# Performance work log

Measured on AMD Instinct MI355X. Metric: run time of the kernel, lower is better.

## Reference

```python
import jax, jax.numpy as jnp
import numpy as np
from jax import lax

# fixed differential-operator kernel bank K() from SPDE_pac (8 channels of 3x3 stencils)
_K = np.zeros((8, 3, 3), np.float32)
_K[0, 1, 1] = 1.0
_K[1, 1, 1] = 2.0
_K[2, 1, 0] = -1.0; _K[2, 1, 2] = -1.0
_K[3, 1, 1] = 2.0
_K[4, 0, 1] = -1.0; _K[4, 2, 1] = -1.0
_K[5, 0, 0] = -0.5; _K[5, 2, 2] = -0.5; _K[5, 0, 2] = 0.5; _K[5, 2, 0] = 0.5
_K[6, 1, 0] = -1.0; _K[6, 1, 2] = 1.0
_K[7, 0, 1] = 1.0; _K[7, 2, 1] = -1.0
_KMAT = jnp.asarray(_K)


def _conv(x, w):
    # 3x3 same-padded conv, no bias (torch Conv2d padding=1, bias=False)
    return lax.conv_general_dilated(x, w, (1, 1), 'SAME',
                                    dimension_numbers=('NCHW', 'OIHW', 'NCHW'))


def _softplus10(x):
    return jax.nn.softplus(10.0 * x) / 10.0


def _forward(x, conv1_w, conv2_w, conv3_w, pac_w, pac_b):
    b, t, h, w = x.shape
    # ---- encode_param_CNN ----
    p = _conv(jax.nn.relu(x), conv1_w)
    p = _conv(jax.nn.relu(p), conv2_w)
    params = _conv(p, conv3_w)                       # [b, 6t, h, w]
    # ---- decode_param_CNN (kept in [b,t,h,w] layout; H = gamma*I + v v^T per pixel) ----
    kappa = _softplus10(params[:, :t])
    m1d = params[:, t:2 * t]                         # decoder m1 -> m[:,0]
    m2d = params[:, 2 * t:3 * t]                     # decoder m2 -> m[:,1]
    gamma = _softplus10(params[:, 3 * t:4 * t])
    vx = params[:, 4 * t:5 * t]
    vy = params[:, 5 * t:6 * t]
    H11 = gamma + vx * vx
    H22 = gamma + vy * vy
    H12 = vx * vy
    # ---- SPDE_pac kernel construction ----
    # guide channels as in source: (kappa, H11, 1/H11, H22, 1/H22, H12, m[:,1], m[:,0])
    guide = jnp.stack([kappa, H11, 1.0 / H11, H22, 1.0 / H22, H12, m2d, m1d], axis=2)  # [b,t,8,h,w]
    w_ker = jnp.einsum('ide,btihw->btdehw', _KMAT, guide)   # [b,t,3,3,h,w]
    w_ker = w_ker.at[:, :, 1, 1].add(1.0)                   # w_I identity-center kernel
    # ---- pixel-adaptive conv; loop over k is independent (reads x[:,k+1]) -> vectorize over time ----
    xin = x[:, 1:]                                          # [b,t-1,h,w]
    xp = jnp.pad(xin, ((0, 0), (0, 0), (1, 1), (1, 1)))
    patches = jnp.stack([xp[:, :, d:d + h, e:e + w]
                         for d in range(3) for e in range(3)], axis=2)  # [b,t-1,9,h,w]
    wflat = w_ker[:, 1:].reshape(b, t - 1, 9, h, w)
    out = jnp.einsum('k,btkhw,btkhw->bthw', pac_w.reshape(9), wflat, patches) + pac_b[0]
    # last time slice of x_spde is never written -> zeros
    return jnp.concatenate([out, jnp.zeros((b, 1, h, w), x.dtype)], axis=1)


def setup_inputs() -> dict:
    key = jax.random.key(0)
    ks = jax.random.split(key, 6)
    b, t, h, w = 4, 10, 256, 256
    dim_ae = 32
    x = jax.random.normal(ks[0], (b, t, h, w), jnp.float32)
    conv1_w = jax.random.normal(ks[1], (dim_ae, t, 3, 3), jnp.float32) * 0.05
    conv2_w = jax.random.normal(ks[2], (2 * dim_ae, dim_ae, 3, 3), jnp.float32) * 0.05
    conv3_w = jax.random.normal(ks[3], (6 * t, 2 * dim_ae, 3, 3), jnp.float32) * 0.05
    pac_w = jax.random.normal(ks[4], (1, 1, 3, 3), jnp.float32) * 0.2
    pac_b = jax.random.normal(ks[5], (1,), jnp.float32) * 0.1
    return {"x": x, "conv1_w": conv1_w, "conv2_w": conv2_w,
            "conv3_w": conv3_w, "pac_w": pac_w, "pac_b": pac_b}


def reference(x, conv1_w, conv2_w, conv3_w, pac_w, pac_b):
    return _forward(x, conv1_w, conv2_w, conv3_w, pac_w, pac_b)
```

## Files before the change

kernel.cpp:

```cpp
#include <hip/hip_runtime.h>
#include <math.h>

#define HH 256
#define WW 256
#define HW (HH * WW)
#define TB 10

typedef __attribute__((ext_vector_type(4))) float f32x4;
typedef __attribute__((ext_vector_type(8))) short s16x8;

__device__ __forceinline__ float sp10(float x) {
    float z = 10.0f * x;
    return (fmaxf(z, 0.0f) + log1pf(expf(-fabsf(z)))) * 0.1f;
}

__device__ __forceinline__ unsigned short f2bf(float f) {
    unsigned u = __float_as_uint(f);
    u = u + 0x7FFFu + ((u >> 16) & 1u);
    return (unsigned short)(u >> 16);
}
__device__ __forceinline__ void bsplit(float v, unsigned short& h, unsigned short& l) {
    h = f2bf(v);
    float hf = __uint_as_float(((unsigned)h) << 16);
    l = f2bf(v - hf);
}
__device__ __forceinline__ unsigned pk(unsigned short a, unsigned short b) {
    return (unsigned)a | ((unsigned)b << 16);
}
__device__ __forceinline__ void sp2(float a, float b, unsigned& uh, unsigned& ul) {
    unsigned short h1, l1, h2, l2;
    bsplit(a, h1, l1); bsplit(b, h2, l2);
    uh = pk(h1, h2); ul = pk(l1, l2);
}

__global__ __launch_bounds__(256) void prep_weights(
    const float* __restrict__ w1, const float* __restrict__ w2,
    const float* __restrict__ w3,
    float* __restrict__ wt1,
    unsigned short* __restrict__ wA2h, unsigned short* __restrict__ wA2l,
    unsigned short* __restrict__ wA3h, unsigned short* __restrict__ wA3l)
{
    int idx = blockIdx.x * 256 + threadIdx.x;
    if (idx < 2880) {
        int ci = idx / 288; int rem = idx - ci * 288;
        int tap = rem / 32; int co = rem - tap * 32;
        wt1[idx] = w1[co * 90 + ci * 9 + tap];
    }
    if (idx < 18432) {
        int t = idx / 2048; int rem = idx - t * 2048;
        int co = rem >> 5; int ci = rem & 31;
        unsigned short h, l;
        bsplit(w2[(co * 32 + ci) * 9 + t], h, l);
        wA2h[idx] = h; wA2l[idx] = l;
    }
    if (idx < 36864) {
        int t = idx / 4096; int rem = idx - t * 4096;
        int co = rem >> 6; int ci = rem & 63;
        float v = 0.0f;
        if (co < 54) {
            int tt = co / 6 + 1;
            int g  = co - (tt - 1) * 6;
            v = w3[((g * 10 + tt) * 64 + ci) * 9 + t];
        }
        unsigned short h, l;
        bsplit(v, h, l);
        wA3h[idx] = h; wA3l[idx] = l;
    }
}

__global__ __launch_bounds__(256, 4) void conv1_k(
    const float* __restrict__ x, const float* __restrict__ wt1,
    unsigned short* __restrict__ q1h, unsigned short* __restrict__ q1l)
{
    __shared__ float tile[10 * 612];
    const int tx = threadIdx.x & 15, ty = threadIdx.x >> 4;
    const int h0 = blockIdx.y * 32, w0 = blockIdx.x * 16;
    const int b = blockIdx.z;
    const float* inb = x + (size_t)b * TB * HW;

    float acc0[32], acc1[32];
#pragma unroll
    for (int c = 0; c < 32; ++c) { acc0[c] = 0.0f; acc1[c] = 0.0f; }

    for (int i = threadIdx.x; i < 10 * 612; i += 256) {
        int ci = i / 612; int r = i - ci * 612;
        int row = r / 18; int col = r - row * 18;
        int gy = h0 + row - 1, gx = w0 + col - 1;
        float v = 0.0f;
        if (gy >= 0 && gy < HH && gx >= 0 && gx < WW)
            v = fmaxf(inb[(size_t)ci * HW + gy * WW + gx], 0.0f);
        tile[i] = v;
    }
    __syncthreads();

    for (int ci = 0; ci < 10; ++ci) {
        const float* tp = &tile[ci * 612 + (2 * ty) * 18 + tx];
        float v[12];
#pragma unroll
        for (int r = 0; r < 4; ++r)
#pragma unroll
            for (int c = 0; c < 3; ++c)
                v[r * 3 + c] = tp[r * 18 + c];
        const float* wp = wt1 + ci * 288;
#pragma unroll
        for (int t = 0; t < 9; ++t) {
            float a0 = v[t], a1 = v[t + 3];
#pragma unroll
            for (int c = 0; c < 32; ++c) {
                float wv = wp[t * 32 + c];
                acc0[c] = fmaf(wv, a0, acc0[c]);
                acc1[c] = fmaf(wv, a1, acc1[c]);
            }
        }
    }

    const int h = h0 + 2 * ty, w = w0 + tx;
    const size_t q1base = (size_t)b * HW * 32;
#pragma unroll
    for (int p = 0; p < 2; ++p) {
        const float* src = p ? acc1 : acc0;
        size_t off = q1base + ((size_t)(h + p) * WW + w) * 32;
#pragma unroll
        for (int g = 0; g < 4; ++g) {
            uint4 Uh, Ul;
            sp2(fmaxf(src[g*8+0],0.f), fmaxf(src[g*8+1],0.f), Uh.x, Ul.x);
            sp2(fmaxf(src[g*8+2],0.f), fmaxf(src[g*8+3],0.f), Uh.y, Ul.y);
            sp2(fmaxf(src[g*8+4],0.f), fmaxf(src[g*8+5],0.f), Uh.z, Ul.z);
            sp2(fmaxf(src[g*8+6],0.f), fmaxf(src[g*8+7],0.f), Uh.w, Ul.w);
            *(uint4*)(q1h + off + g * 8) = Uh;
            *(uint4*)(q1l + off + g * 8) = Ul;
        }
    }
}

__global__ __launch_bounds__(256, 2) void conv2_mfma(
    const unsigned short* __restrict__ q1h, const unsigned short* __restrict__ q1l,
    const unsigned short* __restrict__ wA2h, const unsigned short* __restrict__ wA2l,
    unsigned short* __restrict__ q2h, unsigned short* __restrict__ q2l)
{
    __shared__ short lds[18 * 18 * 72];
    const int tid = threadIdx.x;
    const int lane = tid & 63, wave = tid >> 6;
    const int px = lane & 15, quad = lane >> 4;
    const int h0 = blockIdx.y * 16, w0 = blockIdx.x * 16, b = blockIdx.z;

    for (int i = tid; i < 648; i += 256) {
        int plane = (i >= 324) ? 1 : 0;
        int rc = i - plane * 324;
        int row = rc / 18, col = rc - row * 18;
        int gy = h0 + row - 1, gx = w0 + col - 1;
        uint4 v0 = {0,0,0,0}, v1 = v0, v2 = v0, v3 = v0;
        if (gy >= 0 && gy < HH && gx >= 0 && gx < WW) {
            const uint4* gp = (const uint4*)((plane ? q1l : q1h)
                + (size_t)b * HW * 32 + ((size_t)gy * WW + gx) * 32);
            v0 = gp[0]; v1 = gp[1]; v2 = gp[2]; v3 = gp[3];
        }
        uint4* dp = (uint4*)&lds[(row * 18 + col) * 72 + plane * 32];
        dp[0] = v0; dp[1] = v1; dp[2] = v2; dp[3] = v3;
    }
    __syncthreads();

    f32x4 acc[4][4];
#pragma unroll
    for (int r = 0; r < 4; ++r)
#pragma unroll
        for (int ct = 0; ct < 4; ++ct)
            acc[r][ct] = (f32x4){0.f, 0.f, 0.f, 0.f};

#pragma unroll
    for (int t = 0; t < 9; ++t) {
        const int dy = t / 3, dx = t - 3 * (t / 3);
        s16x8 ah[4], al[4];
#pragma unroll
        for (int ct = 0; ct < 4; ++ct) {
            int wb = (t * 64 + ct * 16 + px) * 32 + quad * 8;
            ah[ct] = *(const s16x8*)(wA2h + wb);
            al[ct] = *(const s16x8*)(wA2l + wb);
        }
#pragma unroll
        for (int r = 0; r < 4; ++r) {
            int py = wave * 4 + r;
            const short* bp = &lds[((py + dy) * 18 + (px + dx)) * 72 + quad * 8];
            s16x8 bh = *(const s16x8*)bp;
            s16x8 bl = *(const s16x8*)(bp + 32);
#pragma unroll
            for (int ct = 0; ct < 4; ++ct) {
                acc[r][ct] = __builtin_amdgcn_mfma_f32_16x16x32_bf16(ah[ct], bh, acc[r][ct], 0, 0, 0);
                acc[r][ct] = __builtin_amdgcn_mfma_f32_16x16x32_bf16(ah[ct], bl, acc[r][ct], 0, 0, 0);
                acc[r][ct] = __builtin_amdgcn_mfma_f32_16x16x32_bf16(al[ct], bh, acc[r][ct], 0, 0, 0);
            }
        }
    }

#pragma unroll
    for (int r = 0; r < 4; ++r) {
        int py = wave * 4 + r;
        size_t pix = (size_t)b * HW + (size_t)(h0 + py) * WW + (w0 + px);
#pragma unroll
        for (int ct = 0; ct < 4; ++ct) {
            int co0 = ct * 16 + quad * 4;
            uint2 Uh, Ul;
            sp2(acc[r][ct][0], acc[r][ct][1], Uh.x, Ul.x);
            sp2(acc[r][ct][2], acc[r][ct][3], Uh.y, Ul.y);
            size_t off = pix * 64 + co0;
            *(uint2*)(q2h + off) = Uh;
            *(uint2*)(q2l + off) = Ul;
        }
    }
}

#define PSTR 260
__global__ __launch_bounds__(256, 2) void conv3_mfma(
    const unsigned short* __restrict__ q2h, const unsigned short* __restrict__ q2l,
    const unsigned short* __restrict__ wA3h, const unsigned short* __restrict__ wA3l,
    const float* __restrict__ x, const float* __restrict__ pacw,
    const float* __restrict__ pacb, float* __restrict__ out)
{
    __shared__ float smem[14080];
    short* lds = (short*)smem;
    const int tid = threadIdx.x;
    const int lane = tid & 63, wave = tid >> 6;
    const int px = lane & 15, quad = lane >> 4;
    const int h0 = blockIdx.y * 16, w0 = blockIdx.x * 16, b = blockIdx.z;

    f32x4 acc[4][4];
#pragma unroll
    for (int r = 0; r < 4; ++r)
#pragma unroll
        for (int ct = 0; ct < 4; ++ct)
            acc[r][ct] = (f32x4){0.f, 0.f, 0.f, 0.f};

    for (int half = 0; half < 2; ++half) {
        __syncthreads();
        for (int i = tid; i < 648; i += 256) {
            int plane = (i >= 324) ? 1 : 0;
            int rc = i - plane * 324;
            int row = rc / 18, col = rc - row * 18;
            int gy = h0 + row - 1, gx = w0 + col - 1;
            uint4 v0 = {0,0,0,0}, v1 = v0, v2 = v0, v3 = v0;
            if (gy >= 0 && gy < HH && gx >= 0 && gx < WW) {
                const uint4* gp = (const uint4*)((plane ? q2l : q2h)
                    + (size_t)b * HW * 64 + ((size_t)gy * WW + gx) * 64 + half * 32);
                v0 = gp[0]; v1 = gp[1]; v2 = gp[2]; v3 = gp[3];
            }
            uint4* dp = (uint4*)&lds[(row * 18 + col) * 72 + plane * 32];
            dp[0] = v0; dp[1] = v1; dp[2] = v2; dp[3] = v3;
        }
        __syncthreads();

#pragma unroll
        for (int t = 0; t < 9; ++t) {
            const int dy = t / 3, dx = t - 3 * (t / 3);
            s16x8 ah[4], al[4];
#pragma unroll
            for (int ct = 0; ct < 4; ++ct) {
                int wb = (t * 64 + ct * 16 + px) * 64 + half * 32 + quad * 8;
                ah[ct] = *(const s16x8*)(wA3h + wb);
                al[ct] = *(const s16x8*)(wA3l + wb);
            }
#pragma unroll
            for (int r = 0; r < 4; ++r) {
                int py = wave * 4 + r;
                const short* bp = &lds[((py + dy) * 18 + (px + dx)) * 72 + quad * 8];
                s16x8 bh = *(const s16x8*)bp;
                s16x8 bl = *(const s16x8*)(bp + 32);
#pragma unroll
                for (int ct = 0; ct < 4; ++ct) {
                    acc[r][ct] = __builtin_amdgcn_mfma_f32_16x16x32_bf16(ah[ct], bh, acc[r][ct], 0, 0, 0);
                    acc[r][ct] = __builtin_amdgcn_mfma_f32_16x16x32_bf16(ah[ct], bl, acc[r][ct], 0, 0, 0);
                    acc[r][ct] = __builtin_amdgcn_mfma_f32_16x16x32_bf16(al[ct], bh, acc[r][ct], 0, 0, 0);
                }
            }
        }
    }

    __syncthreads();
    float* lds2 = smem;
#pragma unroll
    for (int r = 0; r < 4; ++r) {
        int pf = (wave * 4 + r) * 16 + px;
#pragma unroll
        for (int ct = 0; ct < 4; ++ct)
#pragma unroll
            for (int g = 0; g < 4; ++g) {
                int co = ct * 16 + quad * 4 + g;
                if (co < 54) lds2[co * PSTR + pf] = acc[r][ct][g];
            }
    }
    __syncthreads();

    float ac[54];
#pragma unroll
    for (int c = 0; c < 54; ++c) ac[c] = lds2[c * PSTR + tid];

    float pw[9];
#pragma unroll
    for (int k = 0; k < 9; ++k) pw[k] = pacw[k];
    const float pbias = pacb[0];
    const int h = h0 + (tid >> 4), w = w0 + (tid & 15);
    const float* xb = x + (size_t)b * TB * HW;
    float* ob = out + (size_t)b * TB * HW;

#pragma unroll
    for (int j = 0; j < 9; ++j) {
        const int tt = j + 1;
        float kappa = sp10(ac[j * 6 + 0]);
        float m1d   = ac[j * 6 + 1];
        float m2d   = ac[j * 6 + 2];
        float gamma = sp10(ac[j * 6 + 3]);
        float vx    = ac[j * 6 + 4];
        float vy    = ac[j * 6 + 5];
        float H11 = gamma + vx * vx;
        float H22 = gamma + vy * vy;
        float H12 = vx * vy;
        float iH11 = 1.0f / H11;
        float iH22 = 1.0f / H22;
        float wk[9];
        wk[0] = -0.5f * H12;  wk[1] = -iH22 + m1d;  wk[2] = 0.5f * H12;
        wk[3] = -iH11 - m2d;
        wk[4] = kappa + 2.0f * H11 + 2.0f * H22 + 1.0f;
        wk[5] = -iH11 + m2d;
        wk[6] = 0.5f * H12;   wk[7] = -iH22 - m1d;  wk[8] = -0.5f * H12;

        const float* xc = xb + (size_t)tt * HW;
        float s = 0.0f;
#pragma unroll
        for (int dy = 0; dy < 3; ++dy)
#pragma unroll
            for (int dx = 0; dx < 3; ++dx) {
                int gy = h + dy - 1, gx = w + dx - 1;
                float xv = (gy >= 0 && gy < HH && gx >= 0 && gx < WW)
                               ? xc[gy * WW + gx] : 0.0f;
                s = fmaf(pw[dy * 3 + dx] * wk[dy * 3 + dx], xv, s);
            }
        ob[(size_t)j * HW + (size_t)h * WW + w] = s + pbias;
    }
    ob[(size_t)9 * HW + (size_t)h * WW + w] = 0.0f;
}

extern "C" void kernel_launch(void* const* d_in, const int* in_sizes, int n_in,
                              void* d_out, int out_size, void* d_ws, size_t ws_size,
                              hipStream_t stream)
{
    const float* x    = (const float*)d_in[0];
    const float* w1   = (const float*)d_in[1];
    const float* w2   = (const float*)d_in[2];
    const float* w3   = (const float*)d_in[3];
    const float* pacw = (const float*)d_in[4];
    const float* pacb = (const float*)d_in[5];
    float* out = (float*)d_out;
    char* p = (char*)d_ws;

    float* wt1 = (float*)p;
    unsigned short* wA2h = (unsigned short*)(p + 11520);
    unsigned short* wA2l = (unsigned short*)(p + 11520 + 36864);
    unsigned short* wA3h = (unsigned short*)(p + 11520 + 2 * 36864);
    unsigned short* wA3l = (unsigned short*)(p + 11520 + 2 * 36864 + 73728);
    const size_t woff = 11520 + 2 * 36864 + 2 * 73728;

    prep_weights<<<144, 256, 0, stream>>>(w1, w2, w3, wt1, wA2h, wA2l, wA3h, wA3l);

    const size_t q1sz1 = (size_t)HW * 32 * 2;
    const size_t q2sz1 = (size_t)HW * 64 * 2;
    const size_t need_full = woff + 4 * (2 * q1sz1 + 2 * q2sz1);
    dim3 blk(256);

    if (ws_size >= need_full) {
        unsigned short* q1h = (unsigned short*)(p + woff);
        unsigned short* q1l = (unsigned short*)(p + woff + 4 * q1sz1);
        unsigned short* q2h = (unsigned short*)(p + woff + 8 * q1sz1);
        unsigned short* q2l = (unsigned short*)(p + woff + 8 * q1sz1 + 4 * q2sz1);
        conv1_k<<<dim3(16, 8, 4), blk, 0, stream>>>(x, wt1, q1h, q1l);
        conv2_mfma<<<dim3(16, 16, 4), blk, 0, stream>>>(q1h, q1l, wA2h, wA2l, q2h, q2l);
        conv3_mfma<<<dim3(16, 16, 4), blk, 0, stream>>>(q2h, q2l, wA3h, wA3l,
                                                        x, pacw, pacb, out);
    } else {
        unsigned short* q1h = (unsigned short*)(p + woff);
        unsigned short* q1l = (unsigned short*)(p + woff + q1sz1);
        unsigned short* q2h = (unsigned short*)(p + woff + 2 * q1sz1);
        unsigned short* q2l = (unsigned short*)(p + woff + 2 * q1sz1 + q2sz1);
        for (int b = 0; b < 4; ++b) {
            const float* xb = x + (size_t)b * TB * HW;
            float* outb = out + (size_t)b * TB * HW;
            conv1_k<<<dim3(16, 8, 1), blk, 0, stream>>>(xb, wt1, q1h, q1l);
            conv2_mfma<<<dim3(16, 16, 1), blk, 0, stream>>>(q1h, q1l, wA2h, wA2l, q2h, q2l);
            conv3_mfma<<<dim3(16, 16, 1), blk, 0, stream>>>(q2h, q2l, wA3h, wA3l,
                                                            xb, pacw, pacb, outb);
        }
    }
}
```

Baseline: 255.8 us.

## Stage hi/lo planes separately in LDS to raise conv2/conv3 occupancy

The conv2 and conv3 MFMA kernels now stage the high and low bf16 planes into LDS one at a time, which shrinks the shared tile from 72 to 40 shorts per pixel. The launch bound rises to 4 blocks per SM. The split-bf16 product is now done per plane (hi*wh + hi*wl, then lo*wh), keeping the same three MFMAs. The conv3 epilogue transposes accumulators through LDS in two channel chunks instead of holding 54 floats in registers, cutting LDS use and register pressure. The cost is extra __syncthreads and staging passes per block.

```diff
diff --git a/kernel.cpp b/kernel.cpp
--- a/kernel.cpp
+++ b/kernel.cpp
@@ -5,6 +5,7 @@
 #define WW 256
 #define HW (HH * WW)
 #define TB 10
+#define PSTR 260
 
 typedef __attribute__((ext_vector_type(4))) float f32x4;
 typedef __attribute__((ext_vector_type(8))) short s16x8;
@@ -133,33 +134,17 @@
     }
 }
 
-__global__ __launch_bounds__(256, 2) void conv2_mfma(
+__global__ __launch_bounds__(256, 4) void conv2_mfma(
     const unsigned short* __restrict__ q1h, const unsigned short* __restrict__ q1l,
     const unsigned short* __restrict__ wA2h, const unsigned short* __restrict__ wA2l,
     unsigned short* __restrict__ q2h, unsigned short* __restrict__ q2l)
 {
-    __shared__ short lds[18 * 18 * 72];
+    __shared__ short lds[324 * 40];
     const int tid = threadIdx.x;
     const int lane = tid & 63, wave = tid >> 6;
     const int px = lane & 15, quad = lane >> 4;
     const int h0 = blockIdx.y * 16, w0 = blockIdx.x * 16, b = blockIdx.z;
 
-    for (int i = tid; i < 648; i += 256) {
-        int plane = (i >= 324) ? 1 : 0;
-        int rc = i - plane * 324;
-        int row = rc / 18, col = rc - row * 18;
-        int gy = h0 + row - 1, gx = w0 + col - 1;
-        uint4 v0 = {0,0,0,0}, v1 = v0, v2 = v0, v3 = v0;
-        if (gy >= 0 && gy < HH && gx >= 0 && gx < WW) {
-            const uint4* gp = (const uint4*)((plane ? q1l : q1h)
-                + (size_t)b * HW * 32 + ((size_t)gy * WW + gx) * 32);
-            v0 = gp[0]; v1 = gp[1]; v2 = gp[2]; v3 = gp[3];
-        }
-        uint4* dp = (uint4*)&lds[(row * 18 + col) * 72 + plane * 32];
-        dp[0] = v0; dp[1] = v1; dp[2] = v2; dp[3] = v3;
-    }
-    __syncthreads();
-
     f32x4 acc[4][4];
 #pragma unroll
     for (int r = 0; r < 4; ++r)
@@ -168,26 +153,43 @@
             acc[r][ct] = (f32x4){0.f, 0.f, 0.f, 0.f};
 
 #pragma unroll
-    for (int t = 0; t < 9; ++t) {
-        const int dy = t / 3, dx = t - 3 * (t / 3);
-        s16x8 ah[4], al[4];
-#pragma unroll
-        for (int ct = 0; ct < 4; ++ct) {
-            int wb = (t * 64 + ct * 16 + px) * 32 + quad * 8;
-            ah[ct] = *(const s16x8*)(wA2h + wb);
-            al[ct] = *(const s16x8*)(wA2l + wb);
-        }
-#pragma unroll
-        for (int r = 0; r < 4; ++r) {
-            int py = wave * 4 + r;
-            const short* bp = &lds[((py + dy) * 18 + (px + dx)) * 72 + quad * 8];
-            s16x8 bh = *(const s16x8*)bp;
-            s16x8 bl = *(const s16x8*)(bp + 32);
+    for (int plane = 0; plane < 2; ++plane) {
+        if (plane) __syncthreads();
+        const unsigned short* src = plane ? q1l : q1h;
+        for (int i = tid; i < 324; i += 256) {
+            int row = i / 18, col = i - (i / 18) * 18;
+            int gy = h0 + row - 1, gx = w0 + col - 1;
+            uint4 v0 = {0,0,0,0}, v1 = v0, v2 = v0, v3 = v0;
+            if (gy >= 0 && gy < HH && gx >= 0 && gx < WW) {
+                const uint4* gp = (const uint4*)(src
+                    + (size_t)b * HW * 32 + ((size_t)gy * WW + gx) * 32);
+                v0 = gp[0]; v1 = gp[1]; v2 = gp[2]; v3 = gp[3];
+            }
+            uint4* dp = (uint4*)&lds[i * 40];
+            dp[0] = v0; dp[1] = v1; dp[2] = v2; dp[3] = v3;
+        }
+        __syncthreads();
+
+#pragma unroll
+        for (int t = 0; t < 9; ++t) {
+            const int dy = t / 3, dx = t - 3 * (t / 3);
+            s16x8 ah[4], al[4];
 #pragma unroll
             for (int ct = 0; ct < 4; ++ct) {
-                acc[r][ct] = __builtin_amdgcn_mfma_f32_16x16x32_bf16(ah[ct], bh, acc[r][ct], 0, 0, 0);
-                acc[r][ct] = __builtin_amdgcn_mfma_f32_16x16x32_bf16(ah[ct], bl, acc[r][ct], 0, 0, 0);
-                acc[r][ct] = __builtin_amdgcn_mfma_f32_16x16x32_bf16(al[ct], bh, acc[r][ct], 0, 0, 0);
+                int wb = (t * 64 + ct * 16 + px) * 32 + quad * 8;
+                ah[ct] = *(const s16x8*)(wA2h + wb);
+                if (plane == 0) al[ct] = *(const s16x8*)(wA2l + wb);
+            }
+#pragma unroll
+            for (int r = 0; r < 4; ++r) {
+                int py = wave * 4 + r;
+                s16x8 bv = *(const s16x8*)&lds[((py + dy) * 18 + (px + dx)) * 40 + quad * 8];
+#pragma unroll
+                for (int ct = 0; ct < 4; ++ct) {
+                    acc[r][ct] = __builtin_amdgcn_mfma_f32_16x16x32_bf16(ah[ct], bv, acc[r][ct], 0, 0, 0);
+                    if (plane == 0)
+                        acc[r][ct] = __builtin_amdgcn_mfma_f32_16x16x32_bf16(al[ct], bv, acc[r][ct], 0, 0, 0);
+                }
             }
         }
     }
@@ -209,14 +211,13 @@
     }
 }
 
-#define PSTR 260
-__global__ __launch_bounds__(256, 2) void conv3_mfma(
+__global__ __launch_bounds__(256, 4) void conv3_mfma(
     const unsigned short* __restrict__ q2h, const unsigned short* __restrict__ q2l,
     const unsigned short* __restrict__ wA3h, const unsigned short* __restrict__ wA3l,
     const float* __restrict__ x, const float* __restrict__ pacw,
     const float* __restrict__ pacb, float* __restrict__ out)
 {
-    __shared__ float smem[14080];
+    __shared__ float smem[7800];
     short* lds = (short*)smem;
     const int tid = threadIdx.x;
     const int lane = tid & 63, wave = tid >> 6;
@@ -230,68 +231,50 @@
         for (int ct = 0; ct < 4; ++ct)
             acc[r][ct] = (f32x4){0.f, 0.f, 0.f, 0.f};
 
+#pragma unroll
     for (int half = 0; half < 2; ++half) {
-        __syncthreads();
-        for (int i = tid; i < 648; i += 256) {
-            int plane = (i >= 324) ? 1 : 0;
-            int rc = i - plane * 324;
-            int row = rc / 18, col = rc - row * 18;
-            int gy = h0 + row - 1, gx = w0 + col - 1;
-            uint4 v0 = {0,0,0,0}, v1 = v0, v2 = v0, v3 = v0;
-            if (gy >= 0 && gy < HH && gx >= 0 && gx < WW) {
-                const uint4* gp = (const uint4*)((plane ? q2l : q2h)
-                    + (size_t)b * HW * 64 + ((size_t)gy * WW + gx) * 64 + half * 32);
-                v0 = gp[0]; v1 = gp[1]; v2 = gp[2]; v3 = gp[3];
-            }
-            uint4* dp = (uint4*)&lds[(row * 18 + col) * 72 + plane * 32];
-            dp[0] = v0; dp[1] = v1; dp[2] = v2; dp[3] = v3;
-        }
-        __syncthreads();
-
-#pragma unroll
-        for (int t = 0; t < 9; ++t) {
-            const int dy = t / 3, dx = t - 3 * (t / 3);
-            s16x8 ah[4], al[4];
-#pragma unroll
-            for (int ct = 0; ct < 4; ++ct) {
-                int wb = (t * 64 + ct * 16 + px) * 64 + half * 32 + quad * 8;
-                ah[ct] = *(const s16x8*)(wA3h + wb);
-                al[ct] = *(const s16x8*)(wA3l + wb);
-            }
-#pragma unroll
-            for (int r = 0; r < 4; ++r) {
-                int py = wave * 4 + r;
-                const short* bp = &lds[((py + dy) * 18 + (px + dx)) * 72 + quad * 8];
-                s16x8 bh = *(const s16x8*)bp;
-                s16x8 bl = *(const s16x8*)(bp + 32);
+#pragma unroll
+        for (int plane = 0; plane < 2; ++plane) {
+            if (half || plane) __syncthreads();
+            const unsigned short* src = plane ? q2l : q2h;
+            for (int i = tid; i < 324; i += 256) {
+                int row = i / 18, col = i - (i / 18) * 18;
+                int gy = h0 + row - 1, gx = w0 + col - 1;
+                uint4 v0 = {0,0,0,0}, v1 = v0, v2 = v0, v3 = v0;
+                if (gy >= 0 && gy < HH && gx >= 0 && gx < WW) {
+                    const uint4* gp = (const uint4*)(src
+                        + (size_t)b * HW * 64 + ((size_t)gy * WW + gx) * 64 + half * 32);
+                    v0 = gp[0]; v1 = gp[1]; v2 = gp[2]; v3 = gp[3];
+                }
+                uint4* dp = (uint4*)&lds[i * 40];
+                dp[0] = v0; dp[1] = v1; dp[2] = v2; dp[3] = v3;
+            }
+            __syncthreads();
+
+#pragma unroll
+            for (int t = 0; t < 9; ++t) {
+                const int dy = t / 3, dx = t - 3 * (t / 3);
+                s16x8 ah[4], al[4];
 #pragma unroll
                 for (int ct = 0; ct < 4; ++ct) {
-                    acc[r][ct] = __builtin_amdgcn_mfma_f32_16x16x32_bf16(ah[ct], bh, acc[r][ct], 0, 0, 0);
-                    acc[r][ct] = __builtin_amdgcn_mfma_f32_16x16x32_bf16(ah[ct], bl, acc[r][ct], 0, 0, 0);
-                    acc[r][ct] = __builtin_amdgcn_mfma_f32_16x16x32_bf16(al[ct], bh, acc[r][ct], 0, 0, 0);
-                }
-            }
-        }
-    }
-
-    __syncthreads();
-    float* lds2 = smem;
-#pragma unroll
-    for (int r = 0; r < 4; ++r) {
-        int pf = (wave * 4 + r) * 16 + px;
-#pragma unroll
-        for (int ct = 0; ct < 4; ++ct)
-#pragma unroll
-            for (int g = 0; g < 4; ++g) {
-                int co = ct * 16 + quad * 4 + g;
-                if (co < 54) lds2[co * PSTR + pf] = acc[r][ct][g];
-            }
-    }
-    __syncthreads();
-
-    float ac[54];
-#pragma unroll
-    for (int c = 0; c < 54; ++c) ac[c] = lds2[c * PSTR + tid];
+                    int wb = (t * 64 + ct * 16 + px) * 64 + half * 32 + quad * 8;
+                    ah[ct] = *(const s16x8*)(wA3h + wb);
+                    if (plane == 0) al[ct] = *(const s16x8*)(wA3l + wb);
+                }
+#pragma unroll
+                for (int r = 0; r < 4; ++r) {
+                    int py = wave * 4 + r;
+                    s16x8 bv = *(const s16x8*)&lds[((py + dy) * 18 + (px + dx)) * 40 + quad * 8];
+#pragma unroll
+                    for (int ct = 0; ct < 4; ++ct) {
+                        acc[r][ct] = __builtin_amdgcn_mfma_f32_16x16x32_bf16(ah[ct], bv, acc[r][ct], 0, 0, 0);
+                        if (plane == 0)
+                            acc[r][ct] = __builtin_amdgcn_mfma_f32_16x16x32_bf16(al[ct], bv, acc[r][ct], 0, 0, 0);
+                    }
+                }
+            }
+        }
+    }
 
     float pw[9];
 #pragma unroll
@@ -300,41 +283,62 @@
     const int h = h0 + (tid >> 4), w = w0 + (tid & 15);
     const float* xb = x + (size_t)b * TB * HW;
     float* ob = out + (size_t)b * TB * HW;
-
-#pragma unroll
-    for (int j = 0; j < 9; ++j) {
-        const int tt = j + 1;
-        float kappa = sp10(ac[j * 6 + 0]);
-        float m1d   = ac[j * 6 + 1];
-        float m2d   = ac[j * 6 + 2];
-        float gamma = sp10(ac[j * 6 + 3]);
-        float vx    = ac[j * 6 + 4];
-        float vy    = ac[j * 6 + 5];
-        float H11 = gamma + vx * vx;
-        float H22 = gamma + vy * vy;
-        float H12 = vx * vy;
-        float iH11 = 1.0f / H11;
-        float iH22 = 1.0f / H22;
-        float wk[9];
-        wk[0] = -0.5f * H12;  wk[1] = -iH22 + m1d;  wk[2] = 0.5f * H12;
-        wk[3] = -iH11 - m2d;
-        wk[4] = kappa + 2.0f * H11 + 2.0f * H22 + 1.0f;
-        wk[5] = -iH11 + m2d;
-        wk[6] = 0.5f * H12;   wk[7] = -iH22 - m1d;  wk[8] = -0.5f * H12;
-
-        const float* xc = xb + (size_t)tt * HW;
-        float s = 0.0f;
-#pragma unroll
-        for (int dy = 0; dy < 3; ++dy)
-#pragma unroll
-            for (int dx = 0; dx < 3; ++dx) {
-                int gy = h + dy - 1, gx = w + dx - 1;
-                float xv = (gy >= 0 && gy < HH && gx >= 0 && gx < WW)
-                               ? xc[gy * WW + gx] : 0.0f;
-                s = fmaf(pw[dy * 3 + dx] * wk[dy * 3 + dx], xv, s);
-            }
-        ob[(size_t)j * HW + (size_t)h * WW + w] = s + pbias;
-    }
+    const int pf = (wave * 4) * 16;
+
+#pragma unroll
+    for (int chunk = 0; chunk < 2; ++chunk) {
+        const int lo = chunk * 30, hi = chunk ? 54 : 30;
+        __syncthreads();
+#pragma unroll
+        for (int r = 0; r < 4; ++r) {
+            int pfr = (wave * 4 + r) * 16 + px;
+#pragma unroll
+            for (int ct = 0; ct < 4; ++ct)
+#pragma unroll
+                for (int g = 0; g < 4; ++g) {
+                    int co = ct * 16 + quad * 4 + g;
+                    if (co >= lo && co < hi)
+                        smem[(co - lo) * PSTR + pfr] = acc[r][ct][g];
+                }
+        }
+        __syncthreads();
+
+        const int j0 = chunk * 5, j1 = chunk ? 9 : 5;
+        for (int j = j0; j < j1; ++j) {
+            const int cb = j * 6 - lo;
+            float kappa = sp10(smem[(cb + 0) * PSTR + tid]);
+            float m1d   = smem[(cb + 1) * PSTR + tid];
+            float m2d   = smem[(cb + 2) * PSTR + tid];
+            float gamma = sp10(smem[(cb + 3) * PSTR + tid]);
+            float vx    = smem[(cb + 4) * PSTR + tid];
+            float vy    = smem[(cb + 5) * PSTR + tid];
+            float H11 = gamma + vx * vx;
+            float H22 = gamma + vy * vy;
+            float H12 = vx * vy;
+            float iH11 = 1.0f / H11;
+            float iH22 = 1.0f / H22;
+            float wk[9];
+            wk[0] = -0.5f * H12;  wk[1] = -iH22 + m1d;  wk[2] = 0.5f * H12;
+            wk[3] = -iH11 - m2d;
+            wk[4] = kappa + 2.0f * H11 + 2.0f * H22 + 1.0f;
+            wk[5] = -iH11 + m2d;
+            wk[6] = 0.5f * H12;   wk[7] = -iH22 - m1d;  wk[8] = -0.5f * H12;
+
+            const float* xc = xb + (size_t)(j + 1) * HW;
+            float s = 0.0f;
+#pragma unroll
+            for (int dy = 0; dy < 3; ++dy)
+#pragma unroll
+                for (int dx = 0; dx < 3; ++dx) {
+                    int gy = h + dy - 1, gx = w + dx - 1;
+                    float xv = (gy >= 0 && gy < HH && gx >= 0 && gx < WW)
+                                   ? xc[gy * WW + gx] : 0.0f;
+                    s = fmaf(pw[dy * 3 + dx] * wk[dy * 3 + dx], xv, s);
+                }
+            ob[(size_t)j * HW + (size_t)h * WW + w] = s + pbias;
+        }
+    }
+    (void)pf;
     ob[(size_t)9 * HW + (size_t)h * WW + w] = 0.0f;
 }
 
```

Measured after the change: 622.0 us. 143% more time.
